# Kernel tuning notes

Measured on AMD Instinct MI355X. Metric: run time of the kernel, lower is better.

## Reference

```python
import jax, jax.numpy as jnp
import numpy as np

# SLAYER SRM-alpha neuron constants (from network.yaml defaults)
THETA = 10.0      # spike threshold
TAU_S = 10.0      # PSP (srm) time constant
TAU_R = 1.0       # refractory time constant
TS = 1.0          # simulation timestep
TAU_RHO = 1.0     # surrogate gradient width
SCALE_RHO = 1.0   # surrogate gradient scale
E = float(np.e)

@jax.custom_vjp
def spike_fn(v):
    # Heaviside threshold; surrogate gradient in bwd (SLAYER spike pdf)
    return (v >= 0).astype(v.dtype)

def _spike_fwd(v):
    return spike_fn(v), v

def _spike_bwd(v, g):
    sg = (SCALE_RHO / TAU_RHO) * jnp.exp(-jnp.abs(v) / TAU_RHO)
    return (g * sg,)

spike_fn.defvjp(_spike_fwd, _spike_bwd)

def psp_spike(a):
    """SLAYER psp (alpha SRM kernel eps(t)=(t/tau_s)e^{1-t/tau_s}, IIR form)
    followed by spike generation with refractory feedback
    nu(t) = -2*theta*(t/tau_r)e^{1-t/tau_r}. a: [B,C,T] -> spikes [B,C,T].
    Alpha kernels realized exactly as 2-state linear recursions."""
    ds = jnp.exp(jnp.asarray(-TS / TAU_S, a.dtype))
    dr = jnp.exp(jnp.asarray(-TS / TAU_R, a.dtype))
    cs = E / TAU_S
    cr = -2.0 * THETA * E / TAU_R
    B, C, T = a.shape
    z = jnp.zeros((B, C), a.dtype)

    def step(carry, a_t):
        xs, ys, xr, yr = carry
        u = cs * ys + cr * yr          # membrane = psp(a) + refractory
        s = spike_fn(u - THETA)
        xs = ds * xs + a_t             # first-order stage (input)
        ys = ds * (ys + TS * xs)       # alpha stage: ys[t+1]=d*(ys+Ts*xs)
        xr = dr * xr + s               # refractory stages driven by spikes
        yr = dr * (yr + TS * xr)
        return (xs, ys, xr, yr), s

    _, s = jax.lax.scan(step, (z, z, z, z), jnp.moveaxis(a, -1, 0))
    return jnp.moveaxis(s, 0, -1)

def psp(a):
    """Pure SLAYER psp filter (no spiking). a: [B,C,T] -> [B,C,T]."""
    ds = jnp.exp(jnp.asarray(-TS / TAU_S, a.dtype))
    cs = E / TAU_S
    B, C, T = a.shape
    z = jnp.zeros((B, C), a.dtype)

    def step(carry, a_t):
        xs, ys = carry
        p = cs * ys
        xs = ds * xs + a_t
        ys = ds * (ys + TS * xs)
        return (xs, ys), p

    _, p = jax.lax.scan(step, (z, z), jnp.moveaxis(a, -1, 0))
    return jnp.moveaxis(p, 0, -1)

def setup_inputs() -> dict:
    key = jax.random.key(0)
    k1, k2, k3 = jax.random.split(key, 3)
    B, NIN, H, NOUT, T = 64, 4, 512, 2, 2000
    # sparse binary input spike trains, rate ~0.1
    spikeInput = (jax.random.uniform(k1, (B, NIN, T)) < 0.1).astype(jnp.float32)
    W1 = 2.0 * jax.random.normal(k2, (H, NIN), jnp.float32)
    W2 = 2.0 * jax.random.normal(k3, (NOUT, H), jnp.float32)
    return {"spikeInput": spikeInput, "W1": W1, "W2": W2}

def reference(spikeInput, W1, W2):
    # fc1 -> psp -> spike
    s1 = psp_spike(jnp.einsum('oi,bit->bot', W1, spikeInput))
    # fc2 -> psp -> spike
    s2 = psp_spike(jnp.einsum('oh,bht->bot', W2, s1))
    # final psp readout
    return psp(s2)
```

## Files before the change

### kernel.cpp

```cpp
#include <hip/hip_runtime.h>
#include <cstdint>
#include <cstddef>

#define THETA_F 10.0f
#define DS_C 0.9048374180359595731642491f
#define DR_C 0.3678794411714423215955238f
#define CS_C 0.2718281828459045235360287f
#define CR_C -54.3656365691809047072057f
#define P100_C 4.5399929762484854e-05f
#define QC100_C 4.1079555325e-03f

typedef unsigned int       u32;
typedef unsigned long long u64;
typedef unsigned short     u16;

#define W32_WORDS_PER_B  (62 * 512)
#define TAIL_BYTE_OFF    (64 * 62 * 512 * 4)

__global__ __launch_bounds__(128) void k1_layer1(
    const float* __restrict__ inp,
    const float* __restrict__ W1,
    u32* __restrict__ w32, u16* __restrict__ tail16)
{
    __shared__ float table[16 * 128];
    __shared__ alignas(8) unsigned char codes[2048];

    const int tid = threadIdx.x;
    const int b   = blockIdx.x >> 2;
    const int h   = ((blockIdx.x & 3) << 7) + tid;

    const float w0 = W1[h * 4 + 0];
    const float w1 = W1[h * 4 + 1];
    const float w2 = W1[h * 4 + 2];
    const float w3 = W1[h * 4 + 3];
    for (int c = 0; c < 16; ++c) {
        float v = __fmul_rn(w0, (c & 1) ? 1.0f : 0.0f);
        v = __fadd_rn(v, __fmul_rn(w1, (c & 2) ? 1.0f : 0.0f));
        v = __fadd_rn(v, __fmul_rn(w2, (c & 4) ? 1.0f : 0.0f));
        v = __fadd_rn(v, __fmul_rn(w3, (c & 8) ? 1.0f : 0.0f));
        table[c * 128 + tid] = v;
    }
    for (int t = tid; t < 2000; t += 128) {
        const float v0 = inp[(b * 4 + 0) * 2000 + t];
        const float v1 = inp[(b * 4 + 1) * 2000 + t];
        const float v2 = inp[(b * 4 + 2) * 2000 + t];
        const float v3 = inp[(b * 4 + 3) * 2000 + t];
        codes[t] = (unsigned char)((int)(v0 != 0.0f) | ((int)(v1 != 0.0f) << 1) |
                                   ((int)(v2 != 0.0f) << 2) | ((int)(v3 != 0.0f) << 3));
    }
    if (tid < 48) codes[2000 + tid] = 0;
    __syncthreads();

#define ISSUE(CW, BUF) do {                                                   \
        const u32 lo_ = (u32)(CW), hi_ = (u32)((CW) >> 32);                   \
        BUF[0] = table[((lo_      ) & 15) * 128 + tid];                       \
        BUF[1] = table[((lo_ >>  8) & 15) * 128 + tid];                       \
        BUF[2] = table[((lo_ >> 16) & 15) * 128 + tid];                       \
        BUF[3] = table[((lo_ >> 24) & 15) * 128 + tid];                       \
        BUF[4] = table[((hi_      ) & 15) * 128 + tid];                       \
        BUF[5] = table[((hi_ >>  8) & 15) * 128 + tid];                       \
        BUF[6] = table[((hi_ >> 16) & 15) * 128 + tid];                       \
        BUF[7] = table[((hi_ >> 24) & 15) * 128 + tid];                       \
    } while (0)

#define STEP(AV, BITPOS) do {                                                 \
        const float u_ = __fadd_rn(__fmul_rn(CS_C, ys), __fmul_rn(CR_C, yr)); \
        const bool sp_ = (u_ >= THETA_F);                                     \
        xs = __fadd_rn(__fmul_rn(DS_C, xs), (AV));                            \
        ys = __fmul_rn(DS_C, __fadd_rn(ys, xs));                              \
        const float A_ = __fmul_rn(DR_C, xr);                                 \
        xr = sp_ ? __fadd_rn(A_, 1.0f) : A_;                                  \
        yr = __fmul_rn(DR_C, __fadd_rn(yr, xr));                              \
        bits = sp_ ? (bits | (1u << (BITPOS))) : bits;                        \
    } while (0)

#define STEP8(BUF, J0) do {                                                   \
        _Pragma("unroll")                                                     \
        for (int j_ = 0; j_ < 8; ++j_) STEP(BUF[j_], (J0) + j_);              \
    } while (0)

    float xs = 0.0f, ys = 0.0f, xr = 0.0f, yr = 0.0f;
    u32 bits = 0;
    u32* pw = w32 + (size_t)b * W32_WORDS_PER_B + h;

    float bA[8], bB[8];
    u64 cw = *reinterpret_cast<const u64*>(codes);
    ISSUE(cw, bA);
    u64 c1 = *reinterpret_cast<const u64*>(codes + 8);
    u64 c2 = *reinterpret_cast<const u64*>(codes + 16);
    u64 c3 = *reinterpret_cast<const u64*>(codes + 24);
    u64 c4 = *reinterpret_cast<const u64*>(codes + 32);

    for (int t0 = 0; t0 < 1984; t0 += 32) {
        ISSUE(c1, bB);
        const u64 n1 = *reinterpret_cast<const u64*>(codes + t0 + 40);
        const u64 n2 = *reinterpret_cast<const u64*>(codes + t0 + 48);
        const u64 n3 = *reinterpret_cast<const u64*>(codes + t0 + 56);
        const u64 n4 = *reinterpret_cast<const u64*>(codes + t0 + 64);
        STEP8(bA, 0);
        ISSUE(c2, bA);
        STEP8(bB, 8);
        ISSUE(c3, bB);
        STEP8(bA, 16);
        ISSUE(c4, bA);
        STEP8(bB, 24);
        *pw = bits; pw += 512; bits = 0;
        c1 = n1; c2 = n2; c3 = n3; c4 = n4;
    }
    ISSUE(c1, bB);
    STEP8(bA, 0);
    STEP8(bB, 8);
    tail16[b * 512 + h] = (u16)bits;

#undef STEP8
#undef STEP
#undef ISSUE
}

__global__ __launch_bounds__(256) void k2_fc2(
    const u32* __restrict__ w32, const u16* __restrict__ tail16,
    const float* __restrict__ W2,
    float* __restrict__ a2)
{
    __shared__ float w2s[1024];
    __shared__ u32 stage[4096];

    const int tid = threadIdx.x;
    const int b  = blockIdx.x >> 3;
    const int it = blockIdx.x & 7;

    for (int j = tid; j < 1024; j += 256) w2s[j] = W2[j];
    #pragma unroll
    for (int k = 0; k < 16; ++k) {
        const int l = tid + (k << 8);
        const int gtb = (it << 3) + (l >> 9);
        u32 v = 0;
        if (gtb < 62)       v = w32[((size_t)b * 62 + gtb) * 512 + (l & 511)];
        else if (gtb == 62) v = (u32)tail16[b * 512 + (l & 511)];
        stage[l] = v;
    }
    __syncthreads();

    const int t = (it << 8) + tid;
    if (t < 2000) {
        const u32* srow = stage + ((tid >> 5) << 9);
        const int sh = tid & 31;
        float acc0 = 0.0f, acc1 = 0.0f;
        #pragma unroll 8
        for (int hh = 0; hh < 512; ++hh) {
            const bool on = (srow[hh] >> sh) & 1u;
            acc0 = __fadd_rn(acc0, on ? w2s[hh] : 0.0f);
            acc1 = __fadd_rn(acc1, on ? w2s[512 + hh] : 0.0f);
        }
        a2[(size_t)(b * 2 + 0) * 2000 + t] = acc0;
        a2[(size_t)(b * 2 + 1) * 2000 + t] = acc1;
    }
}

__global__ __launch_bounds__(160) void k3lin(
    const float* __restrict__ in, float* __restrict__ out)
{
    __shared__ float ex[8][20], ey[8][20], sx[8][20], sy[8][20];

    const int tid = threadIdx.x;
    const int lc  = tid / 20;
    const int ck  = tid - lc * 20;
    const int chain = blockIdx.x * 8 + lc;
    const float* segi = in  + (size_t)chain * 2000 + ck * 100;
    float*       sego = out + (size_t)chain * 2000 + ck * 100;

    float X = 0.0f, Y = 0.0f;
    for (int g = 0; g < 25; ++g) {
        float4 q = *reinterpret_cast<const float4*>(segi + 4 * g);
        float z;
        z = __fmul_rn(CS_C, Y); X = __fmaf_rn(DS_C, X, q.x);
        Y = __fmul_rn(DS_C, __fadd_rn(Y, X)); q.x = z;
        z = __fmul_rn(CS_C, Y); X = __fmaf_rn(DS_C, X, q.y);
        Y = __fmul_rn(DS_C, __fadd_rn(Y, X)); q.y = z;
        z = __fmul_rn(CS_C, Y); X = __fmaf_rn(DS_C, X, q.z);
        Y = __fmul_rn(DS_C, __fadd_rn(Y, X)); q.z = z;
        z = __fmul_rn(CS_C, Y); X = __fmaf_rn(DS_C, X, q.w);
        Y = __fmul_rn(DS_C, __fadd_rn(Y, X)); q.w = z;
        *reinterpret_cast<float4*>(sego + 4 * g) = q;
    }
    ex[lc][ck] = X; ey[lc][ck] = Y;
    __syncthreads();

    if (tid < 8) {
        float x = 0.0f, y = 0.0f;
        for (int c = 0; c < 20; ++c) {
            sx[tid][c] = x; sy[tid][c] = y;
            const float xn = __fmaf_rn(P100_C, x, ex[tid][c]);
            const float yn = __fadd_rn(
                __fmaf_rn(QC100_C, x, __fmul_rn(P100_C, y)), ey[tid][c]);
            x = xn; y = yn;
        }
    }
    __syncthreads();

    float xh = sx[lc][ck], yh = sy[lc][ck];
    if (ck != 0) {
        for (int g = 0; g < 25; ++g) {
            float4 q = *reinterpret_cast<const float4*>(sego + 4 * g);
            q.x = __fmaf_rn(CS_C, yh, q.x);
            xh = __fmul_rn(DS_C, xh); yh = __fmul_rn(DS_C, __fadd_rn(yh, xh));
            q.y = __fmaf_rn(CS_C, yh, q.y);
            xh = __fmul_rn(DS_C, xh); yh = __fmul_rn(DS_C, __fadd_rn(yh, xh));
            q.z = __fmaf_rn(CS_C, yh, q.z);
            xh = __fmul_rn(DS_C, xh); yh = __fmul_rn(DS_C, __fadd_rn(yh, xh));
            q.w = __fmaf_rn(CS_C, yh, q.w);
            xh = __fmul_rn(DS_C, xh); yh = __fmul_rn(DS_C, __fadd_rn(yh, xh));
            *reinterpret_cast<float4*>(sego + 4 * g) = q;
        }
    }
}

__global__ __launch_bounds__(256) void k3d_par(
    const float* __restrict__ U,
    float* __restrict__ s2)
{
    const int gid = blockIdx.x * 256 + threadIdx.x;
    const int chain = gid / 20;
    const int ck    = gid - chain * 20;
    const float* Urow = U + (size_t)chain * 2000;

    float xr2 = 0.0f, yr2 = 0.0f;

#define RSTEP(UV) do {                                                        \
        const float u_ = __fadd_rn((UV), __fmul_rn(CR_C, yr2));               \
        const bool sp_ = (u_ >= THETA_F);                                     \
        const float A_ = __fmul_rn(DR_C, xr2);                                \
        xr2 = sp_ ? __fadd_rn(A_, 1.0f) : A_;                                 \
        yr2 = __fmul_rn(DR_C, __fadd_rn(yr2, xr2));                           \
    } while (0)

#define ESTEP(UV, SOUT) do {                                                  \
        const float u_ = __fadd_rn((UV), __fmul_rn(CR_C, yr2));               \
        const bool sp_ = (u_ >= THETA_F);                                     \
        SOUT = sp_ ? 1.0f : 0.0f;                                             \
        const float A_ = __fmul_rn(DR_C, xr2);                                \
        xr2 = sp_ ? __fadd_rn(A_, 1.0f) : A_;                                 \
        yr2 = __fmul_rn(DR_C, __fadd_rn(yr2, xr2));                           \
    } while (0)

    if (ck != 0) {
        const float* wseg = Urow + ck * 100 - 64;
        #pragma unroll
        for (int g = 0; g < 16; ++g) {
            const float4 q = *reinterpret_cast<const float4*>(wseg + 4 * g);
            RSTEP(q.x); RSTEP(q.y); RSTEP(q.z); RSTEP(q.w);
        }
    }

    const float* eseg = Urow + ck * 100;
    float* oseg = s2 + (size_t)chain * 2000 + ck * 100;
    #pragma unroll
    for (int g = 0; g < 25; ++g) {
        const float4 q = *reinterpret_cast<const float4*>(eseg + 4 * g);
        float4 o;
        ESTEP(q.x, o.x); ESTEP(q.y, o.y); ESTEP(q.z, o.z); ESTEP(q.w, o.w);
        *reinterpret_cast<float4*>(oseg + 4 * g) = o;
    }

#undef ESTEP
#undef RSTEP
}

extern "C" void kernel_launch(void* const* d_in, const int* in_sizes, int n_in,
                              void* d_out, int out_size, void* d_ws, size_t ws_size,
                              hipStream_t stream)
{
    const float* inp = (const float*)d_in[0];
    const float* W1  = (const float*)d_in[1];
    const float* W2  = (const float*)d_in[2];
    float* out = (float*)d_out;

    u32*   w32    = (u32*)d_ws;
    u16*   tail16 = (u16*)((char*)d_ws + TAIL_BYTE_OFF);
    float* s2buf  = (float*)d_ws;

    k1_layer1<<<dim3(256), dim3(128), 0, stream>>>(inp, W1, w32, tail16);
    k2_fc2<<<dim3(512), dim3(256), 0, stream>>>(w32, tail16, W2, out);
    k3lin<<<dim3(16), dim3(160), 0, stream>>>(out, out);
    k3d_par<<<dim3(10), dim3(256), 0, stream>>>(out, s2buf);
    k3lin<<<dim3(16), dim3(160), 0, stream>>>(s2buf, out);
}
```

Baseline: 155.4 us.

## Fuse layer-2 psp, spike and readout psp into one shared-memory kernel

Replaces the three tail launches (psp filter, refractory spike generation, readout psp) with a single kernel. Each block keeps four chains' membrane potential in shared memory and stores the intermediate spikes as bytes. This removes two kernel launches and the global-memory round trips for the intermediate potential and spike buffers. Parallelism stays at the same total thread count, split across 32 small blocks, and it relies on larger shared-memory use per block.

Measured after the change: 137.5 us. 1.13x faster.

```diff
diff --git a/kernel.cpp b/kernel.cpp
--- a/kernel.cpp
+++ b/kernel.cpp
@@ -157,39 +157,42 @@
     }
 }
 
-__global__ __launch_bounds__(160) void k3lin(
-    const float* __restrict__ in, float* __restrict__ out)
+__global__ __launch_bounds__(80) void k3all(
+    const float* __restrict__ a2, float* __restrict__ out)
 {
-    __shared__ float ex[8][20], ey[8][20], sx[8][20], sy[8][20];
+    __shared__ float U[4][2000];
+    __shared__ unsigned char s2b[4][2000];
+    __shared__ float ex[4][20], ey[4][20], px[4][20], py[4][20];
 
     const int tid = threadIdx.x;
     const int lc  = tid / 20;
     const int ck  = tid - lc * 20;
-    const int chain = blockIdx.x * 8 + lc;
-    const float* segi = in  + (size_t)chain * 2000 + ck * 100;
-    float*       sego = out + (size_t)chain * 2000 + ck * 100;
-
-    float X = 0.0f, Y = 0.0f;
-    for (int g = 0; g < 25; ++g) {
-        float4 q = *reinterpret_cast<const float4*>(segi + 4 * g);
-        float z;
-        z = __fmul_rn(CS_C, Y); X = __fmaf_rn(DS_C, X, q.x);
-        Y = __fmul_rn(DS_C, __fadd_rn(Y, X)); q.x = z;
-        z = __fmul_rn(CS_C, Y); X = __fmaf_rn(DS_C, X, q.y);
-        Y = __fmul_rn(DS_C, __fadd_rn(Y, X)); q.y = z;
-        z = __fmul_rn(CS_C, Y); X = __fmaf_rn(DS_C, X, q.z);
-        Y = __fmul_rn(DS_C, __fadd_rn(Y, X)); q.z = z;
-        z = __fmul_rn(CS_C, Y); X = __fmaf_rn(DS_C, X, q.w);
-        Y = __fmul_rn(DS_C, __fadd_rn(Y, X)); q.w = z;
-        *reinterpret_cast<float4*>(sego + 4 * g) = q;
-    }
-    ex[lc][ck] = X; ey[lc][ck] = Y;
-    __syncthreads();
-
-    if (tid < 8) {
+    const int chain = blockIdx.x * 4 + lc;
+
+    {
+        const float* segi = a2 + (size_t)chain * 2000 + ck * 100;
+        float* segU = &U[lc][ck * 100];
+        float X = 0.0f, Y = 0.0f;
+        for (int g = 0; g < 25; ++g) {
+            float4 qv = *reinterpret_cast<const float4*>(segi + 4 * g);
+            float z;
+            z = __fmul_rn(CS_C, Y); X = __fmaf_rn(DS_C, X, qv.x);
+            Y = __fmul_rn(DS_C, __fadd_rn(Y, X)); qv.x = z;
+            z = __fmul_rn(CS_C, Y); X = __fmaf_rn(DS_C, X, qv.y);
+            Y = __fmul_rn(DS_C, __fadd_rn(Y, X)); qv.y = z;
+            z = __fmul_rn(CS_C, Y); X = __fmaf_rn(DS_C, X, qv.z);
+            Y = __fmul_rn(DS_C, __fadd_rn(Y, X)); qv.z = z;
+            z = __fmul_rn(CS_C, Y); X = __fmaf_rn(DS_C, X, qv.w);
+            Y = __fmul_rn(DS_C, __fadd_rn(Y, X)); qv.w = z;
+            *reinterpret_cast<float4*>(segU + 4 * g) = qv;
+        }
+        ex[lc][ck] = X; ey[lc][ck] = Y;
+    }
+    __syncthreads();
+    if (tid < 4) {
         float x = 0.0f, y = 0.0f;
         for (int c = 0; c < 20; ++c) {
-            sx[tid][c] = x; sy[tid][c] = y;
+            px[tid][c] = x; py[tid][c] = y;
             const float xn = __fmaf_rn(P100_C, x, ex[tid][c]);
             const float yn = __fadd_rn(
                 __fmaf_rn(QC100_C, x, __fmul_rn(P100_C, y)), ey[tid][c]);
@@ -197,35 +200,28 @@
         }
     }
     __syncthreads();
-
-    float xh = sx[lc][ck], yh = sy[lc][ck];
-    if (ck != 0) {
-        for (int g = 0; g < 25; ++g) {
-            float4 q = *reinterpret_cast<const float4*>(sego + 4 * g);
-            q.x = __fmaf_rn(CS_C, yh, q.x);
-            xh = __fmul_rn(DS_C, xh); yh = __fmul_rn(DS_C, __fadd_rn(yh, xh));
-            q.y = __fmaf_rn(CS_C, yh, q.y);
-            xh = __fmul_rn(DS_C, xh); yh = __fmul_rn(DS_C, __fadd_rn(yh, xh));
-            q.z = __fmaf_rn(CS_C, yh, q.z);
-            xh = __fmul_rn(DS_C, xh); yh = __fmul_rn(DS_C, __fadd_rn(yh, xh));
-            q.w = __fmaf_rn(CS_C, yh, q.w);
-            xh = __fmul_rn(DS_C, xh); yh = __fmul_rn(DS_C, __fadd_rn(yh, xh));
-            *reinterpret_cast<float4*>(sego + 4 * g) = q;
-        }
-    }
-}
-
-__global__ __launch_bounds__(256) void k3d_par(
-    const float* __restrict__ U,
-    float* __restrict__ s2)
-{
-    const int gid = blockIdx.x * 256 + threadIdx.x;
-    const int chain = gid / 20;
-    const int ck    = gid - chain * 20;
-    const float* Urow = U + (size_t)chain * 2000;
-
-    float xr2 = 0.0f, yr2 = 0.0f;
-
+    {
+        float xh = px[lc][ck], yh = py[lc][ck];
+        float* segU = &U[lc][ck * 100];
+        if (ck != 0) {
+            for (int g = 0; g < 25; ++g) {
+                float4 qv = *reinterpret_cast<const float4*>(segU + 4 * g);
+                qv.x = __fmaf_rn(CS_C, yh, qv.x);
+                xh = __fmul_rn(DS_C, xh); yh = __fmul_rn(DS_C, __fadd_rn(yh, xh));
+                qv.y = __fmaf_rn(CS_C, yh, qv.y);
+                xh = __fmul_rn(DS_C, xh); yh = __fmul_rn(DS_C, __fadd_rn(yh, xh));
+                qv.z = __fmaf_rn(CS_C, yh, qv.z);
+                xh = __fmul_rn(DS_C, xh); yh = __fmul_rn(DS_C, __fadd_rn(yh, xh));
+                qv.w = __fmaf_rn(CS_C, yh, qv.w);
+                xh = __fmul_rn(DS_C, xh); yh = __fmul_rn(DS_C, __fadd_rn(yh, xh));
+                *reinterpret_cast<float4*>(segU + 4 * g) = qv;
+            }
+        }
+    }
+    __syncthreads();
+
+    {
+        float xr2 = 0.0f, yr2 = 0.0f;
 #define RSTEP(UV) do {                                                        \
         const float u_ = __fadd_rn((UV), __fmul_rn(CR_C, yr2));               \
         const bool sp_ = (u_ >= THETA_F);                                     \
@@ -233,37 +229,68 @@
         xr2 = sp_ ? __fadd_rn(A_, 1.0f) : A_;                                 \
         yr2 = __fmul_rn(DR_C, __fadd_rn(yr2, xr2));                           \
     } while (0)
-
-#define ESTEP(UV, SOUT) do {                                                  \
-        const float u_ = __fadd_rn((UV), __fmul_rn(CR_C, yr2));               \
-        const bool sp_ = (u_ >= THETA_F);                                     \
-        SOUT = sp_ ? 1.0f : 0.0f;                                             \
-        const float A_ = __fmul_rn(DR_C, xr2);                                \
-        xr2 = sp_ ? __fadd_rn(A_, 1.0f) : A_;                                 \
-        yr2 = __fmul_rn(DR_C, __fadd_rn(yr2, xr2));                           \
-    } while (0)
-
-    if (ck != 0) {
-        const float* wseg = Urow + ck * 100 - 64;
-        #pragma unroll
-        for (int g = 0; g < 16; ++g) {
-            const float4 q = *reinterpret_cast<const float4*>(wseg + 4 * g);
-            RSTEP(q.x); RSTEP(q.y); RSTEP(q.z); RSTEP(q.w);
-        }
-    }
-
-    const float* eseg = Urow + ck * 100;
-    float* oseg = s2 + (size_t)chain * 2000 + ck * 100;
-    #pragma unroll
-    for (int g = 0; g < 25; ++g) {
-        const float4 q = *reinterpret_cast<const float4*>(eseg + 4 * g);
-        float4 o;
-        ESTEP(q.x, o.x); ESTEP(q.y, o.y); ESTEP(q.z, o.z); ESTEP(q.w, o.w);
-        *reinterpret_cast<float4*>(oseg + 4 * g) = o;
-    }
-
-#undef ESTEP
+        if (ck != 0) {
+            const float* wseg = &U[lc][ck * 100 - 64];
+            #pragma unroll
+            for (int g = 0; g < 16; ++g) {
+                const float4 qv = *reinterpret_cast<const float4*>(wseg + 4 * g);
+                RSTEP(qv.x); RSTEP(qv.y); RSTEP(qv.z); RSTEP(qv.w);
+            }
+        }
+        const float* eseg = &U[lc][ck * 100];
+        unsigned char* ob = &s2b[lc][ck * 100];
+        for (int g = 0; g < 25; ++g) {
+            const float4 qv = *reinterpret_cast<const float4*>(eseg + 4 * g);
+            const float uv[4] = {qv.x, qv.y, qv.z, qv.w};
+            #pragma unroll
+            for (int j = 0; j < 4; ++j) {
+                const float u_ = __fadd_rn(uv[j], __fmul_rn(CR_C, yr2));
+                const bool sp_ = (u_ >= THETA_F);
+                ob[4 * g + j] = sp_ ? 1 : 0;
+                const float A_ = __fmul_rn(DR_C, xr2);
+                xr2 = sp_ ? __fadd_rn(A_, 1.0f) : A_;
+                yr2 = __fmul_rn(DR_C, __fadd_rn(yr2, xr2));
+            }
+        }
 #undef RSTEP
+    }
+    __syncthreads();
+
+    float* sego = out + (size_t)chain * 2000 + ck * 100;
+    {
+        const unsigned char* si = &s2b[lc][ck * 100];
+        float X = 0.0f, Y = 0.0f;
+        for (int j = 0; j < 100; ++j) {
+            const float a = (float)si[j];
+            const float z = __fmul_rn(CS_C, Y);
+            X = __fmaf_rn(DS_C, X, a);
+            Y = __fmul_rn(DS_C, __fadd_rn(Y, X));
+            sego[j] = z;
+        }
+        ex[lc][ck] = X; ey[lc][ck] = Y;
+    }
+    __syncthreads();
+    if (tid < 4) {
+        float x = 0.0f, y = 0.0f;
+        for (int c = 0; c < 20; ++c) {
+            px[tid][c] = x; py[tid][c] = y;
+            const float xn = __fmaf_rn(P100_C, x, ex[tid][c]);
+            const float yn = __fadd_rn(
+                __fmaf_rn(QC100_C, x, __fmul_rn(P100_C, y)), ey[tid][c]);
+            x = xn; y = yn;
+        }
+    }
+    __syncthreads();
+    {
+        float xh = px[lc][ck], yh = py[lc][ck];
+        if (ck != 0) {
+            for (int j = 0; j < 100; ++j) {
+                sego[j] = __fmaf_rn(CS_C, yh, sego[j]);
+                xh = __fmul_rn(DS_C, xh);
+                yh = __fmul_rn(DS_C, __fadd_rn(yh, xh));
+            }
+        }
+    }
 }
 
 extern "C" void kernel_launch(void* const* d_in, const int* in_sizes, int n_in,
@@ -275,13 +302,10 @@
     const float* W2  = (const float*)d_in[2];
     float* out = (float*)d_out;
 
-    u32*   w32    = (u32*)d_ws;
-    u16*   tail16 = (u16*)((char*)d_ws + TAIL_BYTE_OFF);
-    float* s2buf  = (float*)d_ws;
+    u32* w32    = (u32*)d_ws;
+    u16* tail16 = (u16*)((char*)d_ws + TAIL_BYTE_OFF);
 
     k1_layer1<<<dim3(256), dim3(128), 0, stream>>>(inp, W1, w32, tail16);
     k2_fc2<<<dim3(512), dim3(256), 0, stream>>>(w32, tail16, W2, out);
-    k3lin<<<dim3(16), dim3(160), 0, stream>>>(out, out);
-    k3d_par<<<dim3(10), dim3(256), 0, stream>>>(out, s2buf);
-    k3lin<<<dim3(16), dim3(160), 0, stream>>>(s2buf, out);
+    k3all<<<dim3(32), dim3(80), 0, stream>>>(out, out);
 }
```
